# Performance work log

Hardware: AMD Instinct MI355X
Metric: run time of the kernel (lower is better)

The kernel has to match this reference:

```python
import jax, jax.numpy as jnp
import numpy as np

UNITS = 256
FEAT = 256
NUM_BLOCKS = 4  # start_gru + 2 middle blocks + end_gru
BATCH, T = 128, 384


def _gru_layer(x, kernel, rkernel, bias, return_sequences):
    """Keras GRU (reset_after=True, tanh/sigmoid), zero initial state.
    x: [B,T,D]; kernel: [D,3U]; rkernel: [U,3U]; bias: [2,3U] (input, recurrent).
    Gate order z, r, h as in Keras.
    """
    u = rkernel.shape[0]
    # Precompute input projections for all timesteps (one big GEMM)
    xp = jnp.einsum('btd,dg->btg', x, kernel) + bias[0]  # [B,T,3U]

    def step(h, xt):
        rh = h @ rkernel + bias[1]                 # [B,3U]
        mz, mr, mh = jnp.split(xt, 3, axis=-1)
        rz, rr, rhh = jnp.split(rh, 3, axis=-1)
        z = jax.nn.sigmoid(mz + rz)
        r = jax.nn.sigmoid(mr + rr)
        hh = jnp.tanh(mh + r * rhh)                # reset_after: r applied after recurrent matmul
        h_new = z * h + (1.0 - z) * hh
        return h_new, h_new

    h0 = jnp.zeros((x.shape[0], u), dtype=x.dtype)
    hT, hs = jax.lax.scan(step, h0, jnp.swapaxes(xp, 0, 1))  # scan over time
    return jnp.swapaxes(hs, 0, 1) if return_sequences else hT


def setup_inputs() -> dict:
    key = jax.random.key(0)
    ks = jax.random.split(key, 8)
    s_in = 1.0 / np.sqrt(FEAT)
    s_u = 1.0 / np.sqrt(UNITS)
    x = jax.random.normal(ks[0], (BATCH, T, FEAT), dtype=jnp.float32)
    # first layer params
    k0 = jax.random.normal(ks[1], (FEAT, 3 * UNITS), dtype=jnp.float32) * s_in
    rk0 = jax.random.normal(ks[2], (UNITS, 3 * UNITS), dtype=jnp.float32) * s_u
    b0 = jnp.zeros((2, 3 * UNITS), dtype=jnp.float32)
    # remaining NUM_BLOCKS-1 layers, stacked along leading axis
    L = NUM_BLOCKS - 1
    kern = jax.random.normal(ks[3], (L, UNITS, 3 * UNITS), dtype=jnp.float32) * s_u
    rkern = jax.random.normal(ks[4], (L, UNITS, 3 * UNITS), dtype=jnp.float32) * s_u
    bias = jnp.zeros((L, 2, 3 * UNITS), dtype=jnp.float32)
    return {"x": x, "k0": k0, "rk0": rk0, "b0": b0,
            "kern": kern, "rkern": rkern, "bias": bias}


def reference(x, k0, rk0, b0, kern, rkern, bias):
    # start_gru: return_sequences=True
    h = _gru_layer(x, k0, rk0, b0, return_sequences=True)
    L = kern.shape[0]
    # middle blocks return_sequences=True, last (end_gru) returns final state only
    for i in range(L):
        last = (i == L - 1)
        h = _gru_layer(h, kern[i], rkern[i], bias[i], return_sequences=not last)
    return h  # [B, UNITS]
```

## Files before the change

kernel.cpp:

```cpp
#include <hip/hip_runtime.h>
#include <hip/hip_fp16.h>


#define LAYERS 4
#define TSTEPS 384
#define NCH    8
#define WPL    (48 * 16 * 64 * 8)
#define TILE_STRIDE (16 * 64 * 8)
#define RING   16
#define SLOT_ULL (16 * 128)
#define GRP_ULL  (RING * SLOT_ULL)

typedef _Float16 half8 __attribute__((ext_vector_type(8)));
typedef float    f32x4 __attribute__((ext_vector_type(4)));
typedef unsigned uint4v __attribute__((ext_vector_type(4)));
typedef unsigned long long ull;

#define WP_OFF   0
#define BP_OFF   (LAYERS * WPL * 2)
#define FLAG_OFF (BP_OFF + LAYERS * 1024 * 4)
#define FLAG_BYTES 4096
#define HBUF_OFF (4 * 1024 * 1024)

__global__ void repack_kernel(const float* __restrict__ k0, const float* __restrict__ rk0,
                              const float* __restrict__ b0, const float* __restrict__ kern,
                              const float* __restrict__ rkern, const float* __restrict__ bias,
                              _Float16* __restrict__ Wp, float* __restrict__ Bp)
{
    int idx = blockIdx.x * 256 + threadIdx.x;
    const int total_w = LAYERS * WPL;
    if (idx < total_w) {
        int l = idx / WPL;
        int r = idx - l * WPL;
        int j    = r & 7;
        int lane = (r >> 3) & 63;
        int kt   = (r >> 9) & 15;
        int tile = r >> 13;
        int n = tile * 16 + (lane & 15);
        int k = kt * 32 + (lane >> 4) * 8 + j;
        float v;
        if (l == 0) {
            v = (k < 256) ? k0[(size_t)k * 768 + n] : rk0[(size_t)(k - 256) * 768 + n];
        } else {
            const float* kk = kern  + (size_t)(l - 1) * 256 * 768;
            const float* rk = rkern + (size_t)(l - 1) * 256 * 768;
            v = (k < 256) ? kk[(size_t)k * 768 + n] : rk[(size_t)(k - 256) * 768 + n];
        }
        Wp[idx] = (_Float16)v;
    } else {
        int ib = idx - total_w;
        if (ib < LAYERS * 1024) {
            int l = ib >> 10;
            int i = ib & 1023;
            const float* bs = (l == 0) ? b0 : (bias + (size_t)(l - 1) * 2 * 768);
            float v;
            if (i < 512)      v = bs[i] + bs[768 + i];
            else if (i < 768) v = bs[512 + (i - 512)];
            else              v = bs[768 + 512 + (i - 768)];
            Bp[l * 1024 + i] = v;
        }
    }
}

__launch_bounds__(384, 1)
__global__ void gru_kernel(const float* __restrict__ x,
                           const _Float16* __restrict__ Wp,
                           const float* __restrict__ Bp,
                           ull* __restrict__ hbuf,
                           unsigned int* __restrict__ flags,
                           float* __restrict__ out)
{
    __shared__ _Float16 Af[2][16 * 512];
    __shared__ float    Sc[8][16][17];

    const int tid  = threadIdx.x;
    const int lane = tid & 63;
    const int w    = tid >> 6;
    const int lo16 = lane & 15;
    const int q    = lane >> 4;

    const int s = blockIdx.x & 7;
    const int c = (blockIdx.x >> 3) & 7;
    const int l = blockIdx.x >> 6;
    const int b0row = c * 16;

    const int tile = (w >> 1) * 16 + 2 * s + (w & 1);
    half8 bfrag[16];
    {
        const _Float16* wb = Wp + (size_t)l * WPL + (size_t)tile * TILE_STRIDE;
#pragma unroll
        for (int kt = 0; kt < 16; ++kt)
            bfrag[kt] = *(const half8*)(wb + ((size_t)kt * 64 + lane) * 8);
    }

    const int grow = tid >> 4;
    const int g16  = tid & 15;
    const int gup  = g16 * 2;
    const int ktx  = g16 >> 1;
    const int qq   = (g16 & 1) * 2;
    const int xoff0 = ((ktx * 64) + qq * 16 + grow) * 8;
    const int xoff1 = ((ktx * 64) + (qq + 1) * 16 + grow) * 8;
    const int hoff0 = (((8 + ktx) * 64) + qq * 16 + grow) * 8;
    const int hoff1 = (((8 + ktx) * 64) + (qq + 1) * 16 + grow) * 8;

    float bz[2] = {0,0}, br[2] = {0,0}, bi[2] = {0,0}, bh[2] = {0,0};
    float hprev[2] = {0.f, 0.f};
    if (tid < 256) {
        const float* bp = Bp + l * 1024;
        int ug = s * 32 + gup;
        bz[0] = bp[ug];       bz[1] = bp[ug + 1];
        br[0] = bp[256 + ug]; br[1] = bp[256 + ug + 1];
        bi[0] = bp[512 + ug]; bi[1] = bp[512 + ug + 1];
        bh[0] = bp[768 + ug]; bh[1] = bp[768 + ug + 1];
    }

    unsigned int* fl_own_g = flags + (l * NCH + c) * 16;
    unsigned int* fl_dn_g  = flags + ((l < 3 ? l + 1 : 0) * NCH + c) * 16;
    unsigned int* my_flag  = fl_own_g + s;

    ull*       hb_own = hbuf + (size_t)(l * NCH + c) * GRP_ULL;
    const ull* hb_up  = hbuf + (size_t)((l > 0 ? l - 1 : 0) * NCH + c) * GRP_ULL;

    auto wait_group = [&](const unsigned int* base, unsigned need) {
        for (;;) {
            unsigned v = 0xFFFFFFFFu;
            if (lane < 8)
                v = __hip_atomic_load(base + lane, __ATOMIC_RELAXED,
                                      __HIP_MEMORY_SCOPE_SYSTEM);
            if (__all((int)(v >= need))) return;
            __builtin_amdgcn_s_sleep(1);
        }
    };

    auto stage_x = [&](int t, _Float16* An) {
        if (l == 0) {
            const float* sp = x + ((size_t)(b0row + grow) * TSTEPS + t) * 256 + gup * 8;
            f32x4 a0 = *(const f32x4*)sp,      a1 = *(const f32x4*)(sp + 4);
            f32x4 a2 = *(const f32x4*)(sp + 8), a3 = *(const f32x4*)(sp + 12);
            half8 h0, h1;
            h0[0]=(_Float16)a0[0]; h0[1]=(_Float16)a0[1]; h0[2]=(_Float16)a0[2]; h0[3]=(_Float16)a0[3];
            h0[4]=(_Float16)a1[0]; h0[5]=(_Float16)a1[1]; h0[6]=(_Float16)a1[2]; h0[7]=(_Float16)a1[3];
            h1[0]=(_Float16)a2[0]; h1[1]=(_Float16)a2[1]; h1[2]=(_Float16)a2[2]; h1[3]=(_Float16)a2[3];
            h1[4]=(_Float16)a3[0]; h1[5]=(_Float16)a3[1]; h1[6]=(_Float16)a3[2]; h1[7]=(_Float16)a3[3];
            *(half8*)(An + xoff0) = h0;
            *(half8*)(An + xoff1) = h1;
        } else {
            const ull* spx = hb_up + (size_t)(t & (RING - 1)) * SLOT_ULL + grow * 128 + g16 * 8;
            const unsigned tg = (unsigned)(t + 1);
            ull vx[8];
#pragma unroll
            for (int j = 0; j < 8; ++j)
                vx[j] = __hip_atomic_load(spx + j, __ATOMIC_RELAXED, __HIP_MEMORY_SCOPE_SYSTEM);
            for (;;) {
                bool ok = true;
#pragma unroll
                for (int j = 0; j < 8; ++j)
                    if ((unsigned)(vx[j] >> 32) != tg) {
                        vx[j] = __hip_atomic_load(spx + j, __ATOMIC_RELAXED, __HIP_MEMORY_SCOPE_SYSTEM);
                        ok = false;
                    }
                if (ok) break;
                __builtin_amdgcn_s_sleep(1);
            }
            uint4v w0, w1;
            w0[0]=(unsigned)vx[0]; w0[1]=(unsigned)vx[1]; w0[2]=(unsigned)vx[2]; w0[3]=(unsigned)vx[3];
            w1[0]=(unsigned)vx[4]; w1[1]=(unsigned)vx[5]; w1[2]=(unsigned)vx[6]; w1[3]=(unsigned)vx[7];
            *(uint4v*)(An + xoff0) = w0;
            *(uint4v*)(An + xoff1) = w1;
        }
    };

    if (tid < 256) {
        stage_x(0, Af[0]);
        uint4v z = {0u, 0u, 0u, 0u};
        *(uint4v*)(Af[0] + hoff0) = z;
        *(uint4v*)(Af[0] + hoff1) = z;
    }

    ull vh[8];

    for (int t = 0; t < TSTEPS; ++t) {
        _Float16* A  = Af[t & 1];
        _Float16* An = Af[(t + 1) & 1];

        if (t > 0 && tid < 256) {
            const ull* sph = hb_own + (size_t)((t - 1) & (RING - 1)) * SLOT_ULL + grow * 128 + g16 * 8;
            const unsigned tg = (unsigned)t;
            for (;;) {
                bool ok = true;
#pragma unroll
                for (int j = 0; j < 8; ++j)
                    if ((unsigned)(vh[j] >> 32) != tg) {
                        vh[j] = __hip_atomic_load(sph + j, __ATOMIC_RELAXED, __HIP_MEMORY_SCOPE_SYSTEM);
                        ok = false;
                    }
                if (ok) break;
            }
            uint4v w0, w1;
            w0[0]=(unsigned)vh[0]; w0[1]=(unsigned)vh[1]; w0[2]=(unsigned)vh[2]; w0[3]=(unsigned)vh[3];
            w1[0]=(unsigned)vh[4]; w1[1]=(unsigned)vh[5]; w1[2]=(unsigned)vh[6]; w1[3]=(unsigned)vh[7];
            *(uint4v*)(A + hoff0) = w0;
            *(uint4v*)(A + hoff1) = w1;
        }
        __syncthreads();

        f32x4 acc0 = {0,0,0,0}, acc1 = {0,0,0,0};
#pragma unroll
        for (int kt = 0; kt < 16; ++kt) {
            half8 a = *(const half8*)(A + ((kt * 64) + lane) * 8);
            if (w < 4 || kt < 8)
                acc0 = __builtin_amdgcn_mfma_f32_16x16x32_f16(a, bfrag[kt], acc0, 0, 0, 0);
            else
                acc1 = __builtin_amdgcn_mfma_f32_16x16x32_f16(a, bfrag[kt], acc1, 0, 0, 0);
        }
#pragma unroll
        for (int r = 0; r < 4; ++r) Sc[w][q * 4 + r][lo16] = acc0[r];
        if (w >= 4) {
#pragma unroll
            for (int r = 0; r < 4; ++r) Sc[w + 2][q * 4 + r][lo16] = acc1[r];
        }
        __syncthreads();

        if (l < 3 && t >= RING) wait_group(fl_dn_g, (unsigned)(t - RING + 1));

        if (tid < 256) {
            float hn[2];
#pragma unroll
            for (int j = 0; j < 2; ++j) {
                int u   = gup + j;
                int ut  = u >> 4;
                int col = u & 15;
                float zp = Sc[ut][grow][col]     + bz[j];
                float rp = Sc[2 + ut][grow][col] + br[j];
                float ip = Sc[4 + ut][grow][col] + bi[j];
                float hp = Sc[6 + ut][grow][col] + bh[j];
                float z  = 1.f / (1.f + __expf(-zp));
                float rr = 1.f / (1.f + __expf(-rp));
                float pre = ip + rr * hp;
                float e  = __expf(2.f * pre);
                float th = 1.f - 2.f / (e + 1.f);
                hn[j] = z * hprev[j] + (1.f - z) * th;
                hprev[j] = hn[j];
            }
            union { _Float16 h[2]; unsigned u32; } pk;
            pk.h[0] = (_Float16)hn[0];
            pk.h[1] = (_Float16)hn[1];
            ull word = ((ull)(unsigned)(t + 1) << 32) | (ull)pk.u32;
            __hip_atomic_store(hb_own + (size_t)(t & (RING - 1)) * SLOT_ULL + grow * 128 + s * 16 + g16,
                               word, __ATOMIC_RELAXED, __HIP_MEMORY_SCOPE_SYSTEM);
            if (l == 3 && t == TSTEPS - 1) {
                float* op = out + (size_t)(b0row + grow) * 256 + s * 32 + gup;
                op[0] = hn[0];
                op[1] = hn[1];
            }
        }

        if (t + 1 < TSTEPS && tid < 256) {
            stage_x(t + 1, An);
            const ull* sph = hb_own + (size_t)(t & (RING - 1)) * SLOT_ULL + grow * 128 + g16 * 8;
#pragma unroll
            for (int j = 0; j < 8; ++j)
                vh[j] = __hip_atomic_load(sph + j, __ATOMIC_RELAXED, __HIP_MEMORY_SCOPE_SYSTEM);
        }
        __syncthreads();

        if (tid == 0)
            __hip_atomic_store(my_flag, (unsigned)(t + 1),
                               __ATOMIC_RELAXED, __HIP_MEMORY_SCOPE_SYSTEM);
    }
}

extern "C" void kernel_launch(void* const* d_in, const int* in_sizes, int n_in,
                              void* d_out, int out_size, void* d_ws, size_t ws_size,
                              hipStream_t stream)
{
    const float* x     = (const float*)d_in[0];
    const float* k0    = (const float*)d_in[1];
    const float* rk0   = (const float*)d_in[2];
    const float* b0    = (const float*)d_in[3];
    const float* kern  = (const float*)d_in[4];
    const float* rkern = (const float*)d_in[5];
    const float* bias  = (const float*)d_in[6];
    float* out = (float*)d_out;

    char* ws = (char*)d_ws;
    _Float16*     Wp    = (_Float16*)(ws + WP_OFF);
    float*        Bp    = (float*)(ws + BP_OFF);
    unsigned int* flags = (unsigned int*)(ws + FLAG_OFF);
    ull*          hbuf  = (ull*)(ws + HBUF_OFF);

    hipMemsetAsync(flags, 0, FLAG_BYTES, stream);

    const int total = LAYERS * WPL + LAYERS * 1024;
    repack_kernel<<<(total + 255) / 256, 256, 0, stream>>>(k0, rk0, b0, kern, rkern, bias, Wp, Bp);

    gru_kernel<<<LAYERS * NCH * 8, 384, 0, stream>>>(x, Wp, Bp, hbuf, flags, out);
}
```

Measured before the change: 1.653 ms.

## Merge x/h polling, drop per-step barrier, pad LDS, agent-scope loads, remap blocks

Restructures the per-timestep loop of the persistent GRU kernel. The upstream-x and own-h spin waits become one combined poll loop. The third __syncthreads per step is removed by using a single LDS A buffer, and the step flag is now published right after the MFMA phase. The LDS A tile gets padded strides to avoid bank conflicts. Polling loads switch to agent scope, falling back to system scope after 64 rounds. Block index mapping swaps c and s, which changes CU placement. Together these aim to cut per-step synchronization latency on the serial critical path. They risk visibility or correctness issues from the weaker scope and the earlier flag store.

```diff
diff --git a/kernel.cpp b/kernel.cpp
--- a/kernel.cpp
+++ b/kernel.cpp
@@ -10,6 +10,8 @@
 #define RING   16
 #define SLOT_ULL (16 * 128)
 #define GRP_ULL  (RING * SLOT_ULL)
+#define KP 552
+#define QP 136
 
 typedef _Float16 half8 __attribute__((ext_vector_type(8)));
 typedef float    f32x4 __attribute__((ext_vector_type(4)));
@@ -70,7 +72,7 @@
                            unsigned int* __restrict__ flags,
                            float* __restrict__ out)
 {
-    __shared__ _Float16 Af[2][16 * 512];
+    __shared__ _Float16 Af[16 * KP];
     __shared__ float    Sc[8][16][17];
 
     const int tid  = threadIdx.x;
@@ -79,8 +81,8 @@
     const int lo16 = lane & 15;
     const int q    = lane >> 4;
 
-    const int s = blockIdx.x & 7;
-    const int c = (blockIdx.x >> 3) & 7;
+    const int c = blockIdx.x & 7;
+    const int s = (blockIdx.x >> 3) & 7;
     const int l = blockIdx.x >> 6;
     const int b0row = c * 16;
 
@@ -98,10 +100,10 @@
     const int gup  = g16 * 2;
     const int ktx  = g16 >> 1;
     const int qq   = (g16 & 1) * 2;
-    const int xoff0 = ((ktx * 64) + qq * 16 + grow) * 8;
-    const int xoff1 = ((ktx * 64) + (qq + 1) * 16 + grow) * 8;
-    const int hoff0 = (((8 + ktx) * 64) + qq * 16 + grow) * 8;
-    const int hoff1 = (((8 + ktx) * 64) + (qq + 1) * 16 + grow) * 8;
+    const int xoff0 = ktx * KP + qq * QP + grow * 8;
+    const int xoff1 = ktx * KP + (qq + 1) * QP + grow * 8;
+    const int hoff0 = (8 + ktx) * KP + qq * QP + grow * 8;
+    const int hoff1 = (8 + ktx) * KP + (qq + 1) * QP + grow * 8;
 
     float bz[2] = {0,0}, br[2] = {0,0}, bi[2] = {0,0}, bh[2] = {0,0};
     float hprev[2] = {0.f, 0.f};
@@ -132,82 +134,88 @@
         }
     };
 
-    auto stage_x = [&](int t, _Float16* An) {
+    ull   vx[8], vh[8];
+    f32x4 px0, px1, px2, px3;
+    int   fb = 0;
+
+    if (tid < 256) {
         if (l == 0) {
-            const float* sp = x + ((size_t)(b0row + grow) * TSTEPS + t) * 256 + gup * 8;
-            f32x4 a0 = *(const f32x4*)sp,      a1 = *(const f32x4*)(sp + 4);
-            f32x4 a2 = *(const f32x4*)(sp + 8), a3 = *(const f32x4*)(sp + 12);
-            half8 h0, h1;
-            h0[0]=(_Float16)a0[0]; h0[1]=(_Float16)a0[1]; h0[2]=(_Float16)a0[2]; h0[3]=(_Float16)a0[3];
-            h0[4]=(_Float16)a1[0]; h0[5]=(_Float16)a1[1]; h0[6]=(_Float16)a1[2]; h0[7]=(_Float16)a1[3];
-            h1[0]=(_Float16)a2[0]; h1[1]=(_Float16)a2[1]; h1[2]=(_Float16)a2[2]; h1[3]=(_Float16)a2[3];
-            h1[4]=(_Float16)a3[0]; h1[5]=(_Float16)a3[1]; h1[6]=(_Float16)a3[2]; h1[7]=(_Float16)a3[3];
-            *(half8*)(An + xoff0) = h0;
-            *(half8*)(An + xoff1) = h1;
+            const float* sp = x + ((size_t)(b0row + grow) * TSTEPS + 0) * 256 + gup * 8;
+            px0 = *(const f32x4*)sp;       px1 = *(const f32x4*)(sp + 4);
+            px2 = *(const f32x4*)(sp + 8); px3 = *(const f32x4*)(sp + 12);
         } else {
-            const ull* spx = hb_up + (size_t)(t & (RING - 1)) * SLOT_ULL + grow * 128 + g16 * 8;
-            const unsigned tg = (unsigned)(t + 1);
-            ull vx[8];
+            const ull* spx = hb_up + (size_t)0 * SLOT_ULL + grow * 128 + g16 * 8;
 #pragma unroll
             for (int j = 0; j < 8; ++j)
-                vx[j] = __hip_atomic_load(spx + j, __ATOMIC_RELAXED, __HIP_MEMORY_SCOPE_SYSTEM);
-            for (;;) {
-                bool ok = true;
-#pragma unroll
-                for (int j = 0; j < 8; ++j)
-                    if ((unsigned)(vx[j] >> 32) != tg) {
-                        vx[j] = __hip_atomic_load(spx + j, __ATOMIC_RELAXED, __HIP_MEMORY_SCOPE_SYSTEM);
-                        ok = false;
+                vx[j] = __hip_atomic_load(spx + j, __ATOMIC_RELAXED, __HIP_MEMORY_SCOPE_AGENT);
+        }
+    }
+
+    for (int t = 0; t < TSTEPS; ++t) {
+        if (tid < 256) {
+            const ull* spx = hb_up  + (size_t)(t & (RING - 1)) * SLOT_ULL + grow * 128 + g16 * 8;
+            const ull* sph = hb_own + (size_t)((t - 1) & (RING - 1)) * SLOT_ULL + grow * 128 + g16 * 8;
+            const unsigned xt = (unsigned)(t + 1);
+            const unsigned ht = (unsigned)t;
+            if (l > 0 || t > 0) {
+                int rounds = 0;
+                for (;;) {
+                    bool ok = true;
+                    if (l > 0) {
+#pragma unroll
+                        for (int j = 0; j < 8; ++j)
+                            if ((unsigned)(vx[j] >> 32) != xt) {
+                                vx[j] = fb ? __hip_atomic_load(spx + j, __ATOMIC_RELAXED, __HIP_MEMORY_SCOPE_SYSTEM)
+                                           : __hip_atomic_load(spx + j, __ATOMIC_RELAXED, __HIP_MEMORY_SCOPE_AGENT);
+                                ok = false;
+                            }
                     }
-                if (ok) break;
-                __builtin_amdgcn_s_sleep(1);
-            }
-            uint4v w0, w1;
-            w0[0]=(unsigned)vx[0]; w0[1]=(unsigned)vx[1]; w0[2]=(unsigned)vx[2]; w0[3]=(unsigned)vx[3];
-            w1[0]=(unsigned)vx[4]; w1[1]=(unsigned)vx[5]; w1[2]=(unsigned)vx[6]; w1[3]=(unsigned)vx[7];
-            *(uint4v*)(An + xoff0) = w0;
-            *(uint4v*)(An + xoff1) = w1;
-        }
-    };
-
-    if (tid < 256) {
-        stage_x(0, Af[0]);
-        uint4v z = {0u, 0u, 0u, 0u};
-        *(uint4v*)(Af[0] + hoff0) = z;
-        *(uint4v*)(Af[0] + hoff1) = z;
-    }
-
-    ull vh[8];
-
-    for (int t = 0; t < TSTEPS; ++t) {
-        _Float16* A  = Af[t & 1];
-        _Float16* An = Af[(t + 1) & 1];
-
-        if (t > 0 && tid < 256) {
-            const ull* sph = hb_own + (size_t)((t - 1) & (RING - 1)) * SLOT_ULL + grow * 128 + g16 * 8;
-            const unsigned tg = (unsigned)t;
-            for (;;) {
-                bool ok = true;
-#pragma unroll
-                for (int j = 0; j < 8; ++j)
-                    if ((unsigned)(vh[j] >> 32) != tg) {
-                        vh[j] = __hip_atomic_load(sph + j, __ATOMIC_RELAXED, __HIP_MEMORY_SCOPE_SYSTEM);
-                        ok = false;
+                    if (t > 0) {
+#pragma unroll
+                        for (int j = 0; j < 8; ++j)
+                            if ((unsigned)(vh[j] >> 32) != ht) {
+                                vh[j] = fb ? __hip_atomic_load(sph + j, __ATOMIC_RELAXED, __HIP_MEMORY_SCOPE_SYSTEM)
+                                           : __hip_atomic_load(sph + j, __ATOMIC_RELAXED, __HIP_MEMORY_SCOPE_AGENT);
+                                ok = false;
+                            }
                     }
-                if (ok) break;
-            }
-            uint4v w0, w1;
-            w0[0]=(unsigned)vh[0]; w0[1]=(unsigned)vh[1]; w0[2]=(unsigned)vh[2]; w0[3]=(unsigned)vh[3];
-            w1[0]=(unsigned)vh[4]; w1[1]=(unsigned)vh[5]; w1[2]=(unsigned)vh[6]; w1[3]=(unsigned)vh[7];
-            *(uint4v*)(A + hoff0) = w0;
-            *(uint4v*)(A + hoff1) = w1;
+                    if (ok) break;
+                    if (++rounds >= 64) fb = 1;
+                }
+            }
+            if (l == 0) {
+                half8 h0, h1;
+                h0[0]=(_Float16)px0[0]; h0[1]=(_Float16)px0[1]; h0[2]=(_Float16)px0[2]; h0[3]=(_Float16)px0[3];
+                h0[4]=(_Float16)px1[0]; h0[5]=(_Float16)px1[1]; h0[6]=(_Float16)px1[2]; h0[7]=(_Float16)px1[3];
+                h1[0]=(_Float16)px2[0]; h1[1]=(_Float16)px2[1]; h1[2]=(_Float16)px2[2]; h1[3]=(_Float16)px2[3];
+                h1[4]=(_Float16)px3[0]; h1[5]=(_Float16)px3[1]; h1[6]=(_Float16)px3[2]; h1[7]=(_Float16)px3[3];
+                *(half8*)(Af + xoff0) = h0;
+                *(half8*)(Af + xoff1) = h1;
+            } else {
+                uint4v w0, w1;
+                w0[0]=(unsigned)vx[0]; w0[1]=(unsigned)vx[1]; w0[2]=(unsigned)vx[2]; w0[3]=(unsigned)vx[3];
+                w1[0]=(unsigned)vx[4]; w1[1]=(unsigned)vx[5]; w1[2]=(unsigned)vx[6]; w1[3]=(unsigned)vx[7];
+                *(uint4v*)(Af + xoff0) = w0;
+                *(uint4v*)(Af + xoff1) = w1;
+            }
+            if (t > 0) {
+                uint4v w0, w1;
+                w0[0]=(unsigned)vh[0]; w0[1]=(unsigned)vh[1]; w0[2]=(unsigned)vh[2]; w0[3]=(unsigned)vh[3];
+                w1[0]=(unsigned)vh[4]; w1[1]=(unsigned)vh[5]; w1[2]=(unsigned)vh[6]; w1[3]=(unsigned)vh[7];
+                *(uint4v*)(Af + hoff0) = w0;
+                *(uint4v*)(Af + hoff1) = w1;
+            } else {
+                uint4v z = {0u, 0u, 0u, 0u};
+                *(uint4v*)(Af + hoff0) = z;
+                *(uint4v*)(Af + hoff1) = z;
+            }
         }
         __syncthreads();
 
         f32x4 acc0 = {0,0,0,0}, acc1 = {0,0,0,0};
 #pragma unroll
         for (int kt = 0; kt < 16; ++kt) {
-            half8 a = *(const half8*)(A + ((kt * 64) + lane) * 8);
+            half8 a = *(const half8*)(Af + kt * KP + q * QP + lo16 * 8);
             if (w < 4 || kt < 8)
                 acc0 = __builtin_amdgcn_mfma_f32_16x16x32_f16(a, bfrag[kt], acc0, 0, 0, 0);
             else
@@ -220,6 +228,10 @@
             for (int r = 0; r < 4; ++r) Sc[w + 2][q * 4 + r][lo16] = acc1[r];
         }
         __syncthreads();
+
+        if (tid == 0)
+            __hip_atomic_store(my_flag, (unsigned)(t + 1),
+                               __ATOMIC_RELAXED, __HIP_MEMORY_SCOPE_SYSTEM);
 
         if (l < 3 && t >= RING) wait_group(fl_dn_g, (unsigned)(t - RING + 1));
 
@@ -256,17 +268,21 @@
         }
 
         if (t + 1 < TSTEPS && tid < 256) {
-            stage_x(t + 1, An);
+            if (l == 0) {
+                const float* sp = x + ((size_t)(b0row + grow) * TSTEPS + (t + 1)) * 256 + gup * 8;
+                px0 = *(const f32x4*)sp;       px1 = *(const f32x4*)(sp + 4);
+                px2 = *(const f32x4*)(sp + 8); px3 = *(const f32x4*)(sp + 12);
+            } else {
+                const ull* spx = hb_up + (size_t)((t + 1) & (RING - 1)) * SLOT_ULL + grow * 128 + g16 * 8;
+#pragma unroll
+                for (int j = 0; j < 8; ++j)
+                    vx[j] = __hip_atomic_load(spx + j, __ATOMIC_RELAXED, __HIP_MEMORY_SCOPE_AGENT);
+            }
             const ull* sph = hb_own + (size_t)(t & (RING - 1)) * SLOT_ULL + grow * 128 + g16 * 8;
 #pragma unroll
             for (int j = 0; j < 8; ++j)
-                vh[j] = __hip_atomic_load(sph + j, __ATOMIC_RELAXED, __HIP_MEMORY_SCOPE_SYSTEM);
-        }
-        __syncthreads();
-
-        if (tid == 0)
-            __hip_atomic_store(my_flag, (unsigned)(t + 1),
-                               __ATOMIC_RELAXED, __HIP_MEMORY_SCOPE_SYSTEM);
+                vh[j] = __hip_atomic_load(sph + j, __ATOMIC_RELAXED, __HIP_MEMORY_SCOPE_AGENT);
+        }
     }
 }
 
```

After: 1.934 ms. +17.0%, slower.
